# Kernel tuning notes

Hardware: AMD Instinct MI355X
Metric: run time of the kernel (lower is better)

The kernel has to match this reference:

```python
import jax, jax.numpy as jnp
import numpy as np

FORGET_BIAS = 1.0  # TF LSTMCell default


def _lstm_layer(x_tbd, kernel, bias):
    """x_tbd: [T, B, D]; kernel: [D+H, 4H] (gate order i, j, f, o); returns [T, B, H]."""
    H = kernel.shape[1] // 4
    B = x_tbd.shape[1]
    c0 = jnp.zeros((B, H), dtype=x_tbd.dtype)
    h0 = jnp.zeros((B, H), dtype=x_tbd.dtype)

    def step(carry, x_t):
        c, h = carry
        gates = jnp.concatenate([x_t, h], axis=-1) @ kernel + bias
        i, j, f, o = jnp.split(gates, 4, axis=-1)
        c = jax.nn.sigmoid(f + FORGET_BIAS) * c + jax.nn.sigmoid(i) * jnp.tanh(j)
        h = jax.nn.sigmoid(o) * jnp.tanh(c)
        return (c, h), h

    _, hs = jax.lax.scan(step, (c0, h0), x_tbd)
    return hs


def setup_inputs() -> dict:
    key = jax.random.key(0)
    ks = jax.random.split(key, 4)
    B, T, H, C = 64, 1024, 256, 6
    x = jax.random.normal(ks[0], (B, T, H), dtype=jnp.float32)
    kernel0 = jax.random.normal(ks[1], (2 * H, 4 * H), dtype=jnp.float32) * 0.05
    bias0 = jnp.zeros((4 * H,), dtype=jnp.float32)
    kernel1 = jax.random.normal(ks[2], (2 * H, 4 * H), dtype=jnp.float32) * 0.05
    bias1 = jnp.zeros((4 * H,), dtype=jnp.float32)
    w_out = jax.random.normal(ks[3], (H, C), dtype=jnp.float32)
    b_out = jnp.zeros((C,), dtype=jnp.float32)
    return {"x": x, "kernel0": kernel0, "bias0": bias0,
            "kernel1": kernel1, "bias1": bias1,
            "w_out": w_out, "b_out": b_out}


def reference(x, kernel0, bias0, kernel1, bias1, w_out, b_out):
    # testing=True => keep_prob=1.0 (dropout is identity)
    x_tbd = jnp.transpose(x, (1, 0, 2))        # [T, B, D]
    h1 = _lstm_layer(x_tbd, kernel0, bias0)    # [T, B, H]
    h2 = _lstm_layer(h1, kernel1, bias1)       # [T, B, H]
    # sequence_length == T for every batch row => gather last timestep
    last = h2[-1]                              # [B, H]
    logits = last @ w_out + b_out              # [B, C]
    output = jax.nn.sigmoid(logits)
    prediction = jnp.where(output > 0.5,
                           jnp.ones_like(output), jnp.zeros_like(output))
    return logits, output, prediction
```

## Files before the change

kernel.cpp:

```cpp
#include <hip/hip_runtime.h>
#include <math.h>


#define BB 64
#define TT 1024
#define HH 256
#define NTHREADS 512
#define FLAG_BYTES 4096
#define HBUF_FLOATS (BB * HH)
#define WT_FLOATS (256 * 4 * 512)
#define WS_NEEDED (FLAG_BYTES + (size_t)6 * HBUF_FLOATS * 4 + (size_t)2 * WT_FLOATS * 4)
#define HROW 576

typedef float f32x4 __attribute__((ext_vector_type(4)));
typedef int   i32x2 __attribute__((ext_vector_type(2)));

__device__ __forceinline__ void coh_store(float* p, float v) {
  __hip_atomic_store(p, v, __ATOMIC_RELAXED, __HIP_MEMORY_SCOPE_AGENT);
}
__device__ __forceinline__ void coh_store_i(int* p, int v) {
  __hip_atomic_store(p, v, __ATOMIC_RELAXED, __HIP_MEMORY_SCOPE_AGENT);
}

__device__ __forceinline__ void coh_load4(
    const float* p0, const float* p1, const float* p2, const float* p3,
    f32x4& a0, f32x4& a1, f32x4& a2, f32x4& a3) {
  asm volatile(
      "global_load_dwordx4 %0, %4, off sc0 sc1\n\t"
      "global_load_dwordx4 %1, %5, off sc0 sc1\n\t"
      "global_load_dwordx4 %2, %6, off sc0 sc1\n\t"
      "global_load_dwordx4 %3, %7, off sc0 sc1\n\t"
      "s_waitcnt vmcnt(0)"
      : "=&v"(a0), "=&v"(a1), "=&v"(a2), "=&v"(a3)
      : "v"(p0), "v"(p1), "v"(p2), "v"(p3)
      : "memory");
}

__global__ void transpose_w(const float* __restrict__ src, float* __restrict__ dst) {
  __shared__ float t[64][65];
  const int g  = blockIdx.x;
  const int kt = blockIdx.y;
  const int ut = blockIdx.z;
  const int tx = threadIdx.x & 63;
  const int ty = threadIdx.x >> 6;
  #pragma unroll
  for (int r = ty; r < 64; r += 4)
    t[r][tx] = src[(size_t)(kt * 64 + r) * 1024 + g * 256 + ut * 64 + tx];
  __syncthreads();
  #pragma unroll
  for (int r = ty; r < 64; r += 4)
    dst[((size_t)(ut * 64 + r) * 4 + g) * 512 + kt * 64 + tx] = t[tx][r];
}

__global__ __launch_bounds__(NTHREADS, 2) void lstm2_persistent(
    const float* __restrict__ x,
    const float* __restrict__ b0, const float* __restrict__ b1,
    const float* __restrict__ wt0, const float* __restrict__ wt1,
    float* __restrict__ h1buf, float* __restrict__ h2buf,
    int* __restrict__ flags)
{
  __shared__ float hstage[16 * HROW];
  __shared__ f32x4 part[128 * 17];

  const int blk   = blockIdx.x;
  const int taskB = blk >= 128;
  const int tblk  = taskB ? blk - 128 : blk;
  const int bgrp  = tblk >> 5;
  const int ublk  = tblk & 31;

  const int tid  = threadIdx.x;
  const int lane = tid & 63;
  const int ul   = tid & 7;
  const int kq   = (tid >> 3) & 15;
  const int bt   = tid >> 7;
  const int cS   = tid & 127;
  const int rS   = tid >> 7;
  const int dposS = cS * 4 + (cS >> 3) * 4;
  const bool evenW = (cS < 64);

  const float* WT   = taskB ? wt1 : wt0;
  const float* bias = taskB ? b1 : b0;

  f32x4 w[4][8];
  {
    const float* wb = WT + (size_t)(ublk * 8 + ul) * 2048 + kq * 32;
    #pragma unroll
    for (int g = 0; g < 4; ++g)
      #pragma unroll
      for (int cc = 0; cc < 8; ++cc)
        w[g][cc] = *(const f32x4*)(wb + g * 512 + cc * 4);
  }

  float bi = 0.f, bj = 0.f, bfv = 0.f, bo = 0.f;
  if (tid < 128) {
    const int u = ublk * 8 + (tid & 7);
    bi  = bias[u];
    bj  = bias[256 + u];
    bfv = bias[512 + u];
    bo  = bias[768 + u];
  }
  float cst = 0.f;

  int* myflag = flags + ((size_t)bgrp * 64 + (taskB ? 32 : 0) + ublk) * 2;
  const size_t rstep = (size_t)4 * TT * HH;

  if (!taskB && evenW) {
    const float* bx = x + ((size_t)(bgrp * 16 + rS) * TT + 0) * HH + lane * 4;
    f32x4 v0 = *(const f32x4*)(bx);
    f32x4 v1 = *(const f32x4*)(bx + rstep);
    f32x4 v2 = *(const f32x4*)(bx + 2 * rstep);
    f32x4 v3 = *(const f32x4*)(bx + 3 * rstep);
    *(f32x4*)&hstage[(rS + 0)  * HROW + dposS] = v0;
    *(f32x4*)&hstage[(rS + 4)  * HROW + dposS] = v1;
    *(f32x4*)&hstage[(rS + 8)  * HROW + dposS] = v2;
    *(f32x4*)&hstage[(rS + 12) * HROW + dposS] = v3;
  }

  for (int s = 0; s <= TT + 1; ++s) {
    const bool active = taskB ? (s >= 2) : (s < TT);

    if (active) {
      if (!evenW) {
        const float* src = taskB
            ? (h2buf + (size_t)((s + 1) & 1) * HBUF_FLOATS)
            : (h1buf + (size_t)((s - 1) & 3) * HBUF_FLOATS);
        const float* p0 = src + (size_t)(bgrp * 16 + rS) * HH + lane * 4;
        f32x4 v0, v1, v2, v3;
        coh_load4(p0, p0 + 4 * HH, p0 + 8 * HH, p0 + 12 * HH, v0, v1, v2, v3);
        *(f32x4*)&hstage[(rS + 0)  * HROW + dposS] = v0;
        *(f32x4*)&hstage[(rS + 4)  * HROW + dposS] = v1;
        *(f32x4*)&hstage[(rS + 8)  * HROW + dposS] = v2;
        *(f32x4*)&hstage[(rS + 12) * HROW + dposS] = v3;
      }
      __syncthreads();

      float acc[4][4];
      #pragma unroll
      for (int b4 = 0; b4 < 4; ++b4)
        #pragma unroll
        for (int g = 0; g < 4; ++g) acc[b4][g] = 0.f;

      const int kbase = kq * 36;
      #pragma unroll
      for (int b4 = 0; b4 < 4; ++b4) {
        const float* hp = &hstage[(bt * 4 + b4) * HROW + kbase];
        #pragma unroll
        for (int cc = 0; cc < 8; ++cc) {
          const f32x4 h4 = *(const f32x4*)(hp + cc * 4);
          #pragma unroll
          for (int g = 0; g < 4; ++g) {
            acc[b4][g] = fmaf(h4[0], w[g][cc][0], acc[b4][g]);
            acc[b4][g] = fmaf(h4[1], w[g][cc][1], acc[b4][g]);
            acc[b4][g] = fmaf(h4[2], w[g][cc][2], acc[b4][g]);
            acc[b4][g] = fmaf(h4[3], w[g][cc][3], acc[b4][g]);
          }
        }
      }

      #pragma unroll
      for (int b4 = 0; b4 < 4; ++b4) {
        f32x4 p = { acc[b4][0], acc[b4][1], acc[b4][2], acc[b4][3] };
        part[((bt * 4 + b4) * 8 + ul) * 17 + kq] = p;
      }
      __syncthreads();

      if (tid < 128) {
        float gi = bi, gj = bj, gf = bfv, go = bo;
        #pragma unroll
        for (int q = 0; q < 16; ++q) {
          const f32x4 p = part[tid * 17 + q];
          gi += p[0]; gj += p[1]; gf += p[2]; go += p[3];
        }
        const float ig = 1.f / (1.f + expf(-gi));
        const float jt = tanhf(gj);
        const float fg = 1.f / (1.f + expf(-(gf + 1.0f)));
        const float og = 1.f / (1.f + expf(-go));
        cst = fg * cst + ig * jt;
        const float hn = og * tanhf(cst);

        float* hb = taskB
            ? (h2buf + (size_t)(s & 1) * HBUF_FLOATS)
            : (h1buf + (size_t)(s & 3) * HBUF_FLOATS);
        coh_store(hb + (size_t)(bgrp * 16 + (tid >> 3)) * HH + ublk * 8 + (tid & 7), hn);
        asm volatile("s_waitcnt vmcnt(0)" ::: "memory");
      }
    }

    if (s <= TT && tid < 128 && (tid & 63) == 0)
      coh_store_i(myflag + (tid >> 6), s + 1);

    if (evenW) {
      if (!taskB) {
        if (s + 1 < TT) {
          const float* bx = x + ((size_t)(bgrp * 16 + rS) * TT + (s + 1)) * HH + lane * 4;
          f32x4 v0 = *(const f32x4*)(bx);
          f32x4 v1 = *(const f32x4*)(bx + rstep);
          f32x4 v2 = *(const f32x4*)(bx + 2 * rstep);
          f32x4 v3 = *(const f32x4*)(bx + 3 * rstep);
          *(f32x4*)&hstage[(rS + 0)  * HROW + dposS] = v0;
          *(f32x4*)&hstage[(rS + 4)  * HROW + dposS] = v1;
          *(f32x4*)&hstage[(rS + 8)  * HROW + dposS] = v2;
          *(f32x4*)&hstage[(rS + 12) * HROW + dposS] = v3;
        }
      } else {
        if (s >= 1 && s <= TT) {
          const float* p0 = h1buf + (size_t)((s - 1) & 3) * HBUF_FLOATS
                          + (size_t)(bgrp * 16 + rS) * HH + lane * 4;
          f32x4 v0, v1, v2, v3;
          coh_load4(p0, p0 + 4 * HH, p0 + 8 * HH, p0 + 12 * HH, v0, v1, v2, v3);
          *(f32x4*)&hstage[(rS + 0)  * HROW + dposS] = v0;
          *(f32x4*)&hstage[(rS + 4)  * HROW + dposS] = v1;
          *(f32x4*)&hstage[(rS + 8)  * HROW + dposS] = v2;
          *(f32x4*)&hstage[(rS + 12) * HROW + dposS] = v3;
        }
      }
    }

    if (s <= TT) {
      if (tid < 64) {
        const int* fp = flags + ((size_t)bgrp * 64 + tid) * 2;
        for (;;) {
          i32x2 f;
          asm volatile(
              "global_load_dwordx2 %0, %1, off sc0 sc1\n\t"
              "s_waitcnt vmcnt(0)"
              : "=v"(f) : "v"(fp) : "memory");
          const int v = f[0] < f[1] ? f[0] : f[1];
          if (__all(v >= s + 1)) break;
          __builtin_amdgcn_s_sleep(1);
        }
      }
      __syncthreads();
    }
  }
}

__global__ void head_kernel(const float* __restrict__ h2last,
                            const float* __restrict__ w_out,
                            const float* __restrict__ b_out,
                            float* __restrict__ out)
{
  int tid = threadIdx.x;
  if (tid >= 384) return;
  int bb = tid / 6, cc = tid % 6;
  float acc = b_out[cc];
  const float* hr = h2last + bb * HH;
  #pragma unroll 4
  for (int uu = 0; uu < HH; ++uu) acc = fmaf(hr[uu], w_out[uu * 6 + cc], acc);
  out[tid] = acc;
  float sg = 1.f / (1.f + expf(-acc));
  out[384 + tid] = sg;
  out[768 + tid] = (sg > 0.5f) ? 1.f : 0.f;
}

extern "C" void kernel_launch(void* const* d_in, const int* in_sizes, int n_in,
                              void* d_out, int out_size, void* d_ws, size_t ws_size,
                              hipStream_t stream) {
  const float* x     = (const float*)d_in[0];
  const float* k0    = (const float*)d_in[1];
  const float* b0    = (const float*)d_in[2];
  const float* k1    = (const float*)d_in[3];
  const float* b1    = (const float*)d_in[4];
  const float* w_out = (const float*)d_in[5];
  const float* b_out = (const float*)d_in[6];
  float* out = (float*)d_out;

  if (ws_size < WS_NEEDED) return;

  int*   flags = (int*)d_ws;
  float* h1b   = (float*)((char*)d_ws + FLAG_BYTES);
  float* h2b   = h1b + 4 * HBUF_FLOATS;
  float* wt0   = h2b + 2 * HBUF_FLOATS;
  float* wt1   = wt0 + WT_FLOATS;

  hipMemsetAsync(d_ws, 0, FLAG_BYTES + (size_t)6 * HBUF_FLOATS * 4, stream);

  transpose_w<<<dim3(4, 8, 4), 256, 0, stream>>>(k0, wt0);
  transpose_w<<<dim3(4, 8, 4), 256, 0, stream>>>(k1, wt1);

  lstm2_persistent<<<256, NTHREADS, 0, stream>>>(x, b0, b1, wt0, wt1,
                                                 h1b, h2b, flags);

  head_kernel<<<1, 384, 0, stream>>>(h2b + HBUF_FLOATS, w_out, b_out, out);
}
```

Baseline: 4.136 ms.

## Repartition persistent LSTM into 8 batch groups with 16-unit blocks

Changes the per-block work split from 4 batch groups of 16 rows with 8 hidden units per block to 8 batch groups of 8 rows with 16 hidden units per block. Each cross-block sync group shrinks from 64 to 32 blocks, so per-step flag polling and hidden-state staging loads are smaller. Block indices are interleaved so the two layers' blocks sit side by side, and flag polling moves to a different wave. In exchange, each block loads a larger share of the weight matrix per batch row, and the smaller batch tile gives less weight reuse.

```diff
diff --git a/kernel.cpp b/kernel.cpp
--- a/kernel.cpp
+++ b/kernel.cpp
@@ -6,6 +6,8 @@
 #define TT 1024
 #define HH 256
 #define NTHREADS 512
+#define NGRPS 8
+#define GB 8
 #define FLAG_BYTES 4096
 #define HBUF_FLOATS (BB * HH)
 #define WT_FLOATS (256 * 4 * 512)
@@ -22,17 +24,14 @@
   __hip_atomic_store(p, v, __ATOMIC_RELAXED, __HIP_MEMORY_SCOPE_AGENT);
 }
 
-__device__ __forceinline__ void coh_load4(
-    const float* p0, const float* p1, const float* p2, const float* p3,
-    f32x4& a0, f32x4& a1, f32x4& a2, f32x4& a3) {
+__device__ __forceinline__ void coh_load2(
+    const float* p0, const float* p1, f32x4& a0, f32x4& a1) {
   asm volatile(
-      "global_load_dwordx4 %0, %4, off sc0 sc1\n\t"
-      "global_load_dwordx4 %1, %5, off sc0 sc1\n\t"
-      "global_load_dwordx4 %2, %6, off sc0 sc1\n\t"
-      "global_load_dwordx4 %3, %7, off sc0 sc1\n\t"
+      "global_load_dwordx4 %0, %2, off sc0 sc1\n\t"
+      "global_load_dwordx4 %1, %3, off sc0 sc1\n\t"
       "s_waitcnt vmcnt(0)"
-      : "=&v"(a0), "=&v"(a1), "=&v"(a2), "=&v"(a3)
-      : "v"(p0), "v"(p1), "v"(p2), "v"(p3)
+      : "=&v"(a0), "=&v"(a1)
+      : "v"(p0), "v"(p1)
       : "memory");
 }
 
@@ -59,22 +58,21 @@
     float* __restrict__ h1buf, float* __restrict__ h2buf,
     int* __restrict__ flags)
 {
-  __shared__ float hstage[16 * HROW];
+  __shared__ float hstage[GB * HROW];
   __shared__ f32x4 part[128 * 17];
 
   const int blk   = blockIdx.x;
-  const int taskB = blk >= 128;
-  const int tblk  = taskB ? blk - 128 : blk;
-  const int bgrp  = tblk >> 5;
-  const int ublk  = tblk & 31;
+  const int bgrp  = blk & 7;
+  const int taskB = (blk >> 3) & 1;
+  const int ublk  = blk >> 4;
 
   const int tid  = threadIdx.x;
   const int lane = tid & 63;
-  const int ul   = tid & 7;
-  const int kq   = (tid >> 3) & 15;
-  const int bt   = tid >> 7;
+  const int ul   = tid & 15;
+  const int kq   = (tid >> 4) & 15;
+  const int bt   = tid >> 8;
   const int cS   = tid & 127;
-  const int rS   = tid >> 7;
+  const int rS2  = (tid >> 7) * 2;
   const int dposS = cS * 4 + (cS >> 3) * 4;
   const bool evenW = (cS < 64);
 
@@ -83,7 +81,7 @@
 
   f32x4 w[4][8];
   {
-    const float* wb = WT + (size_t)(ublk * 8 + ul) * 2048 + kq * 32;
+    const float* wb = WT + (size_t)(ublk * 16 + ul) * 2048 + kq * 32;
     #pragma unroll
     for (int g = 0; g < 4; ++g)
       #pragma unroll
@@ -93,7 +91,7 @@
 
   float bi = 0.f, bj = 0.f, bfv = 0.f, bo = 0.f;
   if (tid < 128) {
-    const int u = ublk * 8 + (tid & 7);
+    const int u = ublk * 16 + (tid & 15);
     bi  = bias[u];
     bj  = bias[256 + u];
     bfv = bias[512 + u];
@@ -101,19 +99,15 @@
   }
   float cst = 0.f;
 
-  int* myflag = flags + ((size_t)bgrp * 64 + (taskB ? 32 : 0) + ublk) * 2;
-  const size_t rstep = (size_t)4 * TT * HH;
+  int* myflag = flags + ((size_t)bgrp * 32 + taskB * 16 + ublk) * 2;
+  const size_t bxstep = (size_t)TT * HH;
 
   if (!taskB && evenW) {
-    const float* bx = x + ((size_t)(bgrp * 16 + rS) * TT + 0) * HH + lane * 4;
+    const float* bx = x + ((size_t)(bgrp * GB + rS2) * TT + 0) * HH + cS * 4;
     f32x4 v0 = *(const f32x4*)(bx);
-    f32x4 v1 = *(const f32x4*)(bx + rstep);
-    f32x4 v2 = *(const f32x4*)(bx + 2 * rstep);
-    f32x4 v3 = *(const f32x4*)(bx + 3 * rstep);
-    *(f32x4*)&hstage[(rS + 0)  * HROW + dposS] = v0;
-    *(f32x4*)&hstage[(rS + 4)  * HROW + dposS] = v1;
-    *(f32x4*)&hstage[(rS + 8)  * HROW + dposS] = v2;
-    *(f32x4*)&hstage[(rS + 12) * HROW + dposS] = v3;
+    f32x4 v1 = *(const f32x4*)(bx + bxstep);
+    *(f32x4*)&hstage[(rS2 + 0) * HROW + dposS] = v0;
+    *(f32x4*)&hstage[(rS2 + 1) * HROW + dposS] = v1;
   }
 
   for (int s = 0; s <= TT + 1; ++s) {
@@ -124,13 +118,11 @@
         const float* src = taskB
             ? (h2buf + (size_t)((s + 1) & 1) * HBUF_FLOATS)
             : (h1buf + (size_t)((s - 1) & 3) * HBUF_FLOATS);
-        const float* p0 = src + (size_t)(bgrp * 16 + rS) * HH + lane * 4;
-        f32x4 v0, v1, v2, v3;
-        coh_load4(p0, p0 + 4 * HH, p0 + 8 * HH, p0 + 12 * HH, v0, v1, v2, v3);
-        *(f32x4*)&hstage[(rS + 0)  * HROW + dposS] = v0;
-        *(f32x4*)&hstage[(rS + 4)  * HROW + dposS] = v1;
-        *(f32x4*)&hstage[(rS + 8)  * HROW + dposS] = v2;
-        *(f32x4*)&hstage[(rS + 12) * HROW + dposS] = v3;
+        const float* p0 = src + (size_t)(bgrp * GB + rS2) * HH + (cS & 63) * 4;
+        f32x4 v0, v1;
+        coh_load2(p0, p0 + HH, v0, v1);
+        *(f32x4*)&hstage[(rS2 + 0) * HROW + dposS] = v0;
+        *(f32x4*)&hstage[(rS2 + 1) * HROW + dposS] = v1;
       }
       __syncthreads();
 
@@ -160,7 +152,7 @@
       #pragma unroll
       for (int b4 = 0; b4 < 4; ++b4) {
         f32x4 p = { acc[b4][0], acc[b4][1], acc[b4][2], acc[b4][3] };
-        part[((bt * 4 + b4) * 8 + ul) * 17 + kq] = p;
+        part[((bt * 4 + b4) * 16 + ul) * 17 + kq] = p;
       }
       __syncthreads();
 
@@ -181,7 +173,7 @@
         float* hb = taskB
             ? (h2buf + (size_t)(s & 1) * HBUF_FLOATS)
             : (h1buf + (size_t)(s & 3) * HBUF_FLOATS);
-        coh_store(hb + (size_t)(bgrp * 16 + (tid >> 3)) * HH + ublk * 8 + (tid & 7), hn);
+        coh_store(hb + (size_t)(bgrp * GB + (tid >> 4)) * HH + ublk * 16 + (tid & 15), hn);
         asm volatile("s_waitcnt vmcnt(0)" ::: "memory");
       }
     }
@@ -192,33 +184,27 @@
     if (evenW) {
       if (!taskB) {
         if (s + 1 < TT) {
-          const float* bx = x + ((size_t)(bgrp * 16 + rS) * TT + (s + 1)) * HH + lane * 4;
+          const float* bx = x + ((size_t)(bgrp * GB + rS2) * TT + (s + 1)) * HH + cS * 4;
           f32x4 v0 = *(const f32x4*)(bx);
-          f32x4 v1 = *(const f32x4*)(bx + rstep);
-          f32x4 v2 = *(const f32x4*)(bx + 2 * rstep);
-          f32x4 v3 = *(const f32x4*)(bx + 3 * rstep);
-          *(f32x4*)&hstage[(rS + 0)  * HROW + dposS] = v0;
-          *(f32x4*)&hstage[(rS + 4)  * HROW + dposS] = v1;
-          *(f32x4*)&hstage[(rS + 8)  * HROW + dposS] = v2;
-          *(f32x4*)&hstage[(rS + 12) * HROW + dposS] = v3;
+          f32x4 v1 = *(const f32x4*)(bx + bxstep);
+          *(f32x4*)&hstage[(rS2 + 0) * HROW + dposS] = v0;
+          *(f32x4*)&hstage[(rS2 + 1) * HROW + dposS] = v1;
         }
       } else {
         if (s >= 1 && s <= TT) {
           const float* p0 = h1buf + (size_t)((s - 1) & 3) * HBUF_FLOATS
-                          + (size_t)(bgrp * 16 + rS) * HH + lane * 4;
-          f32x4 v0, v1, v2, v3;
-          coh_load4(p0, p0 + 4 * HH, p0 + 8 * HH, p0 + 12 * HH, v0, v1, v2, v3);
-          *(f32x4*)&hstage[(rS + 0)  * HROW + dposS] = v0;
-          *(f32x4*)&hstage[(rS + 4)  * HROW + dposS] = v1;
-          *(f32x4*)&hstage[(rS + 8)  * HROW + dposS] = v2;
-          *(f32x4*)&hstage[(rS + 12) * HROW + dposS] = v3;
+                          + (size_t)(bgrp * GB + rS2) * HH + cS * 4;
+          f32x4 v0, v1;
+          coh_load2(p0, p0 + HH, v0, v1);
+          *(f32x4*)&hstage[(rS2 + 0) * HROW + dposS] = v0;
+          *(f32x4*)&hstage[(rS2 + 1) * HROW + dposS] = v1;
         }
       }
     }
 
     if (s <= TT) {
-      if (tid < 64) {
-        const int* fp = flags + ((size_t)bgrp * 64 + tid) * 2;
+      if (tid >= 192 && tid < 256) {
+        const int* fp = flags + ((size_t)bgrp * 32 + (lane & 31)) * 2;
         for (;;) {
           i32x2 f;
           asm volatile(
```

Measured after the change: 6.821 ms. 1.65x slower.
